# Kernel optimization log

Hardware: AMD Instinct MI355X
Metric: run time of the kernel (lower is better)

Reference implementation:

```python
import jax, jax.numpy as jnp
import numpy as np

TAU = 100.0
DT = 1.0
NOISE_STD = 0.1
HID = 100


def setup_inputs() -> dict:
    key = jax.random.key(0)
    ks = jax.random.split(key, 7)
    T, B = 750, 1024
    input_seq = jax.random.normal(ks[0], (T, B, 4), dtype=jnp.float32)
    noise = jax.random.normal(ks[1], (T, B, HID), dtype=jnp.float32)
    # orthogonal recurrent weight J [H, H]
    a = jax.random.normal(ks[2], (HID, HID), dtype=jnp.float32)
    q, r = jnp.linalg.qr(a)
    J_w = q * jnp.sign(jnp.diag(r))[None, :]
    # input projection rows [b_m; b_c; b_cm; b_cc] -> [4, H] (xavier for (H,1) fan)
    bound_b = float(np.sqrt(6.0 / (HID + 1)))
    Bmat = jax.random.uniform(ks[3], (4, HID), jnp.float32, -bound_b, bound_b)
    c_x = jnp.zeros((HID,), dtype=jnp.float32)
    bound_w = float(np.sqrt(6.0 / (HID + 1)))
    Wout_w = jax.random.uniform(ks[4], (1, HID), jnp.float32, -bound_w, bound_w)
    Wout_b = jnp.zeros((1,), dtype=jnp.float32)
    return {"input_seq": input_seq, "noise": noise, "J_w": J_w,
            "Bmat": Bmat, "c_x": c_x, "Wout_w": Wout_w, "Wout_b": Wout_b}


def reference(input_seq, noise, J_w, Bmat, c_x, Wout_w, Wout_b):
    # input_seq: [T, B, 4], noise: [T, B, H]
    T, B, _ = input_seq.shape
    alpha = DT / TAU

    # precompute input drive for all steps: u_m@b_m^T + ... == u_t @ Bmat  [T, B, H]
    drive = jnp.einsum('tbi,ih->tbh', input_seq, Bmat)

    def step(x, inp):
        d_t, n_t = inp
        r = jnp.tanh(x)
        dx = alpha * (-x + r @ J_w.T + d_t + c_x + NOISE_STD * n_t)
        x = x + dx
        return x, None

    x0 = jnp.zeros((B, HID), dtype=input_seq.dtype)
    x_final, _ = jax.lax.scan(step, x0, (drive, noise))
    out = jnp.tanh(x_final) @ Wout_w.T + Wout_b  # [B, 1]
    return out.squeeze(-1)  # [B]
```

## Files before the change

kernel.cpp:

```cpp
#include <hip/hip_runtime.h>
#include <hip/hip_bf16.h>

#define HID 100
#define TT 750
#define NBT 1024
#define ALPHA 0.01f
#define NSTD 0.1f

typedef __bf16 bf16x8 __attribute__((ext_vector_type(8)));
typedef __bf16 bf16x4 __attribute__((ext_vector_type(4)));
typedef float floatx4 __attribute__((ext_vector_type(4)));

__device__ __forceinline__ float fast_tanh(float v) {
    float e = __expf(2.0f * v);
    return 1.0f - 2.0f / (e + 1.0f);
}

__global__ __launch_bounds__(448, 2)
void rnn_kernel(const float* __restrict__ useq,
                const float* __restrict__ noise,
                const float* __restrict__ Jw,
                const float* __restrict__ Bm,
                const float* __restrict__ cxp,
                const float* __restrict__ Ww,
                const float* __restrict__ Wb,
                float* __restrict__ out)
{
    __shared__ __align__(16) __bf16 abuf[2][4 * 128];
    __shared__ float red[4][112];

    const int tid  = threadIdx.x;
    const int wv   = tid >> 6;
    const int lane = tid & 63;
    const int m16  = lane & 15;
    const int q    = lane >> 4;
    const int h    = wv * 16 + m16;
    const bool act = (h < HID);
    const int gb0  = blockIdx.x * 4;

    if (tid < 128) ((floatx4*)abuf)[tid] = floatx4{0.f, 0.f, 0.f, 0.f};

    bf16x8 jhi[4], jlo[4];
    #pragma unroll
    for (int s = 0; s < 4; ++s) {
        bf16x8 vh = {}; bf16x8 vl = {};
        #pragma unroll
        for (int j = 0; j < 8; ++j) {
            const int k = s * 32 + q * 8 + j;
            float a = 0.f; bool lo = false;
            if (act) {
                if (k < HID)        { a = Jw[h * HID + k];        lo = true; }
                else if (k < 104)   { a = Bm[(k - 100) * HID + h]; lo = true; }
                else if (k < 108)   { a = Bm[(k - 104) * HID + h]; lo = false; }
                else if (k == 108)  { a = cxp[h];                  lo = true; }
            }
            const __bf16 hi = (__bf16)a;
            vh[j] = hi;
            vl[j] = lo ? (__bf16)(a - (float)hi) : (__bf16)0.f;
        }
        jhi[s] = vh; jlo[s] = vl;
    }

    __syncthreads();

    if (tid < 4) {
        const floatx4 u0 = *(const floatx4*)(useq + (size_t)(gb0 + tid) * 4);
        bf16x4 uh, ul;
        #pragma unroll
        for (int i = 0; i < 4; ++i) {
            const __bf16 hi = (__bf16)u0[i];
            uh[i] = hi; ul[i] = (__bf16)(u0[i] - (float)hi);
        }
        *(bf16x4*)&abuf[0][tid * 128 + ((12 ^ (tid << 2)) << 3) + 4] = uh;
        *(bf16x4*)&abuf[0][tid * 128 + ((13 ^ (tid << 2)) << 3)]     = ul;
        abuf[0][tid * 128 + ((13 ^ (tid << 2)) << 3) + 4] = (__bf16)1.0f;
        abuf[1][tid * 128 + ((13 ^ (tid << 2)) << 3) + 4] = (__bf16)1.0f;
    }

    const float* nptr = noise + (size_t)(gb0 + q) * HID + h;
    float n0 = 0.f, n1 = 0.f, n2 = 0.f, n3 = 0.f;
    if (act) {
        n0 = nptr[(size_t)0 * NBT * HID];
        n1 = nptr[(size_t)1 * NBT * HID];
        n2 = nptr[(size_t)2 * NBT * HID];
        n3 = nptr[(size_t)3 * NBT * HID];
    }
    floatx4 us0 = {}, us1 = {}, us2 = {}, us3 = {};
    if (tid < 4) {
        us1 = *(const floatx4*)(useq + (size_t)1 * NBT * 4 + (gb0 + tid) * 4);
        us2 = *(const floatx4*)(useq + (size_t)2 * NBT * 4 + (gb0 + tid) * 4);
        us3 = *(const floatx4*)(useq + (size_t)3 * NBT * 4 + (gb0 + tid) * 4);
        us0 = *(const floatx4*)(useq + (size_t)4 * NBT * 4 + (gb0 + tid) * 4);
    }

    float x = 0.f;
    __syncthreads();

    auto body = [&](int t, int p, float& nr, floatx4& ur) {
        const int br = m16 >> 2;
        bf16x8 afr[4];
        #pragma unroll
        for (int s = 0; s < 4; ++s) {
            bf16x8 a = {};
            if ((m16 & 3) == 0)
                a = *(const bf16x8*)&abuf[p][br * 128 + ((((s << 2) | q) ^ (br << 2)) << 3)];
            afr[s] = a;
        }
        floatx4 ah = {0.f,0.f,0.f,0.f}, al = {0.f,0.f,0.f,0.f};
        #pragma unroll
        for (int s = 0; s < 4; ++s)
            ah = __builtin_amdgcn_mfma_f32_16x16x32_bf16(afr[s], jhi[s], ah, 0, 0, 0);
        #pragma unroll
        for (int s = 0; s < 4; ++s)
            al = __builtin_amdgcn_mfma_f32_16x16x32_bf16(afr[s], jlo[s], al, 0, 0, 0);
        const float y = ah[0] + al[0];

        if (tid < 4) {
            bf16x4 uh, ul;
            #pragma unroll
            for (int i = 0; i < 4; ++i) {
                const __bf16 hi = (__bf16)ur[i];
                uh[i] = hi; ul[i] = (__bf16)(ur[i] - (float)hi);
            }
            *(bf16x4*)&abuf[p ^ 1][tid * 128 + ((12 ^ (tid << 2)) << 3) + 4] = uh;
            *(bf16x4*)&abuf[p ^ 1][tid * 128 + ((13 ^ (tid << 2)) << 3)]     = ul;
            const int tu = (t + 5 <= TT - 1) ? (t + 5) : (TT - 1);
            ur = *(const floatx4*)(useq + (size_t)tu * NBT * 4 + (gb0 + tid) * 4);
        }

        if (act) {
            x = x * (1.f - ALPHA) + ALPHA * (y + NSTD * nr);
            const float r = fast_tanh(x);
            abuf[p ^ 1][q * 128 + (((h >> 3) ^ (q << 2)) << 3) + (h & 7)] = (__bf16)r;
            const int tn = (t + 4 <= TT - 1) ? (t + 4) : (TT - 1);
            nr = nptr[(size_t)tn * NBT * HID];
        }

        asm volatile("s_waitcnt lgkmcnt(0)\n\ts_barrier" ::: "memory");
    };

    for (int t4 = 0; t4 < 748; t4 += 4) {
        body(t4 + 0, 0, n0, us1);
        body(t4 + 1, 1, n1, us2);
        body(t4 + 2, 0, n2, us3);
        body(t4 + 3, 1, n3, us0);
    }
    body(748, 0, n0, us1);
    body(749, 1, n1, us2);

    if (act) red[q][h] = fast_tanh(x) * Ww[h];
    __syncthreads();
    if (tid < 4) {
        float s = Wb[0];
        #pragma unroll 4
        for (int i = 0; i < HID; ++i) s += red[tid][i];
        out[gb0 + tid] = s;
    }
}

extern "C" void kernel_launch(void* const* d_in, const int* in_sizes, int n_in,
                              void* d_out, int out_size, void* d_ws, size_t ws_size,
                              hipStream_t stream) {
    rnn_kernel<<<dim3(256), dim3(448), 0, stream>>>(
        (const float*)d_in[0], (const float*)d_in[1], (const float*)d_in[2],
        (const float*)d_in[3], (const float*)d_in[4], (const float*)d_in[5],
        (const float*)d_in[6], (float*)d_out);
}
```

Before: 881.3 us.

## Compute input drive in fp32 per thread and split MFMA chains for ILP

```diff
diff --git a/kernel.cpp b/kernel.cpp
--- a/kernel.cpp
+++ b/kernel.cpp
@@ -8,7 +8,6 @@
 #define NSTD 0.1f
 
 typedef __bf16 bf16x8 __attribute__((ext_vector_type(8)));
-typedef __bf16 bf16x4 __attribute__((ext_vector_type(4)));
 typedef float floatx4 __attribute__((ext_vector_type(4)));
 
 __device__ __forceinline__ float fast_tanh(float v) {
@@ -16,7 +15,9 @@
     return 1.0f - 2.0f / (e + 1.0f);
 }
 
-__global__ __launch_bounds__(448, 2)
+#define MFMA(A, B, C) __builtin_amdgcn_mfma_f32_16x16x32_bf16((A), (B), (C), 0, 0, 0)
+
+__global__ __launch_bounds__(448)
 void rnn_kernel(const float* __restrict__ useq,
                 const float* __restrict__ noise,
                 const float* __restrict__ Jw,
@@ -26,7 +27,7 @@
                 const float* __restrict__ Wb,
                 float* __restrict__ out)
 {
-    __shared__ __align__(16) __bf16 abuf[2][4 * 128];
+    __shared__ __align__(16) __bf16 abuf[2][16][128];
     __shared__ float red[4][112];
 
     const int tid  = threadIdx.x;
@@ -38,7 +39,8 @@
     const bool act = (h < HID);
     const int gb0  = blockIdx.x * 4;
 
-    if (tid < 128) ((floatx4*)abuf)[tid] = floatx4{0.f, 0.f, 0.f, 0.f};
+    for (int i = tid; i < 512; i += 448)
+        ((floatx4*)abuf)[i] = floatx4{0.f, 0.f, 0.f, 0.f};
 
     bf16x8 jhi[4], jlo[4];
     #pragma unroll
@@ -47,106 +49,82 @@
         #pragma unroll
         for (int j = 0; j < 8; ++j) {
             const int k = s * 32 + q * 8 + j;
-            float a = 0.f; bool lo = false;
-            if (act) {
-                if (k < HID)        { a = Jw[h * HID + k];        lo = true; }
-                else if (k < 104)   { a = Bm[(k - 100) * HID + h]; lo = true; }
-                else if (k < 108)   { a = Bm[(k - 104) * HID + h]; lo = false; }
-                else if (k == 108)  { a = cxp[h];                  lo = true; }
-            }
+            float a = (act && k < HID) ? Jw[h * HID + k] : 0.0f;
             const __bf16 hi = (__bf16)a;
             vh[j] = hi;
-            vl[j] = lo ? (__bf16)(a - (float)hi) : (__bf16)0.f;
+            vl[j] = (__bf16)(a - (float)hi);
         }
         jhi[s] = vh; jlo[s] = vl;
     }
 
-    __syncthreads();
-
-    if (tid < 4) {
-        const floatx4 u0 = *(const floatx4*)(useq + (size_t)(gb0 + tid) * 4);
-        bf16x4 uh, ul;
-        #pragma unroll
-        for (int i = 0; i < 4; ++i) {
-            const __bf16 hi = (__bf16)u0[i];
-            uh[i] = hi; ul[i] = (__bf16)(u0[i] - (float)hi);
-        }
-        *(bf16x4*)&abuf[0][tid * 128 + ((12 ^ (tid << 2)) << 3) + 4] = uh;
-        *(bf16x4*)&abuf[0][tid * 128 + ((13 ^ (tid << 2)) << 3)]     = ul;
-        abuf[0][tid * 128 + ((13 ^ (tid << 2)) << 3) + 4] = (__bf16)1.0f;
-        abuf[1][tid * 128 + ((13 ^ (tid << 2)) << 3) + 4] = (__bf16)1.0f;
+    float bm0=0.f, bm1=0.f, bm2=0.f, bm3=0.f, cx=0.f;
+    if (act) {
+        bm0 = Bm[0*HID + h]; bm1 = Bm[1*HID + h];
+        bm2 = Bm[2*HID + h]; bm3 = Bm[3*HID + h];
+        cx  = cxp[h];
     }
 
-    const float* nptr = noise + (size_t)(gb0 + q) * HID + h;
-    float n0 = 0.f, n1 = 0.f, n2 = 0.f, n3 = 0.f;
+    const float* nptr = noise + (size_t)(gb0 + q) * HID + (act ? h : (HID - 1));
+    const floatx4* uptr = (const floatx4*)(useq + (size_t)(gb0 + q) * 4);
+    float n0=0.f, n1=0.f, n2=0.f, n3=0.f;
     if (act) {
         n0 = nptr[(size_t)0 * NBT * HID];
         n1 = nptr[(size_t)1 * NBT * HID];
         n2 = nptr[(size_t)2 * NBT * HID];
         n3 = nptr[(size_t)3 * NBT * HID];
     }
-    floatx4 us0 = {}, us1 = {}, us2 = {}, us3 = {};
-    if (tid < 4) {
-        us1 = *(const floatx4*)(useq + (size_t)1 * NBT * 4 + (gb0 + tid) * 4);
-        us2 = *(const floatx4*)(useq + (size_t)2 * NBT * 4 + (gb0 + tid) * 4);
-        us3 = *(const floatx4*)(useq + (size_t)3 * NBT * 4 + (gb0 + tid) * 4);
-        us0 = *(const floatx4*)(useq + (size_t)4 * NBT * 4 + (gb0 + tid) * 4);
-    }
+    floatx4 u0 = uptr[(size_t)0 * NBT];
+    floatx4 u1 = uptr[(size_t)1 * NBT];
+
+    int rdo[4];
+    #pragma unroll
+    for (int s = 0; s < 4; ++s)
+        rdo[s] = m16 * 128 + (((4 * s + q) ^ (m16 & 7)) << 3);
+    const int wro = (4 * q) * 128 + ((((h >> 3) ^ ((4 * q) & 7)) << 3) | (h & 7));
 
     float x = 0.f;
+    const floatx4 kz = {0.f, 0.f, 0.f, 0.f};
     __syncthreads();
 
     auto body = [&](int t, int p, float& nr, floatx4& ur) {
-        const int br = m16 >> 2;
+        const float d = cx + ur[0]*bm0 + ur[1]*bm1 + ur[2]*bm2 + ur[3]*bm3
+                      + NSTD * nr;
+        floatx4 c0 = kz; c0[0] = d;
+
+        const __bf16* ab = &abuf[p][0][0];
         bf16x8 afr[4];
         #pragma unroll
-        for (int s = 0; s < 4; ++s) {
-            bf16x8 a = {};
-            if ((m16 & 3) == 0)
-                a = *(const bf16x8*)&abuf[p][br * 128 + ((((s << 2) | q) ^ (br << 2)) << 3)];
-            afr[s] = a;
-        }
-        floatx4 ah = {0.f,0.f,0.f,0.f}, al = {0.f,0.f,0.f,0.f};
-        #pragma unroll
         for (int s = 0; s < 4; ++s)
-            ah = __builtin_amdgcn_mfma_f32_16x16x32_bf16(afr[s], jhi[s], ah, 0, 0, 0);
-        #pragma unroll
-        for (int s = 0; s < 4; ++s)
-            al = __builtin_amdgcn_mfma_f32_16x16x32_bf16(afr[s], jlo[s], al, 0, 0, 0);
-        const float y = ah[0] + al[0];
+            afr[s] = *(const bf16x8*)(ab + rdo[s]);
 
-        if (tid < 4) {
-            bf16x4 uh, ul;
-            #pragma unroll
-            for (int i = 0; i < 4; ++i) {
-                const __bf16 hi = (__bf16)ur[i];
-                uh[i] = hi; ul[i] = (__bf16)(ur[i] - (float)hi);
-            }
-            *(bf16x4*)&abuf[p ^ 1][tid * 128 + ((12 ^ (tid << 2)) << 3) + 4] = uh;
-            *(bf16x4*)&abuf[p ^ 1][tid * 128 + ((13 ^ (tid << 2)) << 3)]     = ul;
-            const int tu = (t + 5 <= TT - 1) ? (t + 5) : (TT - 1);
-            ur = *(const floatx4*)(useq + (size_t)tu * NBT * 4 + (gb0 + tid) * 4);
-        }
+        floatx4 ah0 = MFMA(afr[1], jhi[1], MFMA(afr[0], jhi[0], c0));
+        floatx4 ah1 = MFMA(afr[3], jhi[3], MFMA(afr[2], jhi[2], kz));
+        floatx4 al0 = MFMA(afr[1], jlo[1], MFMA(afr[0], jlo[0], kz));
+        floatx4 al1 = MFMA(afr[3], jlo[3], MFMA(afr[2], jlo[2], kz));
+        const float y = (ah0[0] + ah1[0]) + (al0[0] + al1[0]);
 
         if (act) {
-            x = x * (1.f - ALPHA) + ALPHA * (y + NSTD * nr);
+            x = x * (1.f - ALPHA) + ALPHA * y;
             const float r = fast_tanh(x);
-            abuf[p ^ 1][q * 128 + (((h >> 3) ^ (q << 2)) << 3) + (h & 7)] = (__bf16)r;
+            abuf[p ^ 1][0][wro] = (__bf16)r;
             const int tn = (t + 4 <= TT - 1) ? (t + 4) : (TT - 1);
             nr = nptr[(size_t)tn * NBT * HID];
         }
-
+        {
+            const int tu = (t + 2 <= TT - 1) ? (t + 2) : (TT - 1);
+            ur = uptr[(size_t)tu * NBT];
+        }
         asm volatile("s_waitcnt lgkmcnt(0)\n\ts_barrier" ::: "memory");
     };
 
     for (int t4 = 0; t4 < 748; t4 += 4) {
-        body(t4 + 0, 0, n0, us1);
-        body(t4 + 1, 1, n1, us2);
-        body(t4 + 2, 0, n2, us3);
-        body(t4 + 3, 1, n3, us0);
+        body(t4 + 0, 0, n0, u0);
+        body(t4 + 1, 1, n1, u1);
+        body(t4 + 2, 0, n2, u0);
+        body(t4 + 3, 1, n3, u1);
     }
-    body(748, 0, n0, us1);
-    body(749, 1, n1, us2);
+    body(748, 0, n0, u0);
+    body(749, 1, n1, u1);
 
     if (act) red[q][h] = fast_tanh(x) * Ww[h];
     __syncthreads();
```

Result: faster. 827.7 us (-6.1%).
